# Kernel optimization log

Measured on AMD Instinct MI355X. Metric: run time of the kernel, lower is better.

The kernel has to match this reference:

```python
import jax, jax.numpy as jnp
import numpy as np

N = 20000      # nodes
E = 320000     # edges (avg degree 16)
NODE_DIM = 64
EDGE_DIM = 32
HID = 128
HEADS = 4
NEG_SLOPE = 0.2


def _gatv2(x, src, dst, edge_attr, Wl, bl, Wr, br, We, att, bias, heads, out_ch):
    """PyG GATv2Conv (concat=True). x:[N,F], src/dst:[E], edge_attr:[E,edge_dim]."""
    n = x.shape[0]
    xl = (x @ Wl + bl).reshape(n, heads, out_ch)          # source transform
    xr = (x @ Wr + br).reshape(n, heads, out_ch)          # target transform
    ee = (edge_attr @ We).reshape(-1, heads, out_ch)      # edge embedding (no bias in PyG)
    m = jax.nn.leaky_relu(xl[src] + xr[dst] + ee, NEG_SLOPE)  # [E,H,C]
    logits = jnp.einsum('ehc,hc->eh', m, att)             # [E,H]
    # segment softmax over incoming edges of each destination node
    lmax = jax.ops.segment_max(logits, dst, num_segments=n)
    ex = jnp.exp(logits - lmax[dst])
    denom = jax.ops.segment_sum(ex, dst, num_segments=n)
    alpha = ex / denom[dst]                               # [E,H]
    out = jax.ops.segment_sum(alpha[..., None] * xl[src], dst, num_segments=n)
    return out.reshape(n, heads * out_ch) + bias


def setup_inputs() -> dict:
    key = jax.random.key(0)
    ks = jax.random.split(key, 24)
    d = {}
    d['x'] = jax.random.normal(ks[0], (N, NODE_DIM), jnp.float32)
    d['edge_index'] = jax.random.randint(ks[1], (2, E), 0, N, jnp.int64)
    d['edge_attr'] = jax.random.normal(ks[2], (E, EDGE_DIM), jnp.float32)
    HC1 = HEADS * HID
    def lin(k, fi, fo):
        return jax.random.normal(k, (fi, fo), jnp.float32) / np.sqrt(fi).astype(np.float32)
    # conv1: node_dim -> hid, heads=4
    d['Wl1'] = lin(ks[3], NODE_DIM, HC1); d['bl1'] = jnp.zeros((HC1,), jnp.float32)
    d['Wr1'] = lin(ks[4], NODE_DIM, HC1); d['br1'] = jnp.zeros((HC1,), jnp.float32)
    d['We1'] = lin(ks[5], EDGE_DIM, HC1)
    d['att1'] = jax.random.normal(ks[6], (HEADS, HID), jnp.float32) / np.sqrt(HID).astype(np.float32)
    d['bias1'] = jnp.zeros((HC1,), jnp.float32)
    # conv2: hid*heads -> hid, heads=1
    d['Wl2'] = lin(ks[7], HC1, HID); d['bl2'] = jnp.zeros((HID,), jnp.float32)
    d['Wr2'] = lin(ks[8], HC1, HID); d['br2'] = jnp.zeros((HID,), jnp.float32)
    d['We2'] = lin(ks[9], EDGE_DIM, HID)
    d['att2'] = jax.random.normal(ks[10], (1, HID), jnp.float32) / np.sqrt(HID).astype(np.float32)
    d['bias2'] = jnp.zeros((HID,), jnp.float32)
    # stereo head
    d['Wh1'] = lin(ks[11], HID, 64); d['bh1'] = jnp.zeros((64,), jnp.float32)
    d['Wh2'] = lin(ks[12], 64, 2);   d['bh2'] = jnp.zeros((2,), jnp.float32)
    return d


def reference(x, edge_index, edge_attr, Wl1, bl1, Wr1, br1, We1, att1, bias1,
              Wl2, bl2, Wr2, br2, We2, att2, bias2, Wh1, bh1, Wh2, bh2):
    src, dst = edge_index[0], edge_index[1]
    h = _gatv2(x, src, dst, edge_attr, Wl1, bl1, Wr1, br1, We1, att1, bias1, HEADS, HID)
    h = jax.nn.relu(h)
    h = _gatv2(h, src, dst, edge_attr, Wl2, bl2, Wr2, br2, We2, att2, bias2, 1, HID)
    h = jax.nn.relu(h @ Wh1 + bh1)
    return h @ Wh2 + bh2  # [N, 2]
```

## Files before the change

kernel.cpp:

```cpp
#include <hip/hip_runtime.h>
#include <hip/hip_bf16.h>
#include <math.h>

#define N_NODES 20000
#define N_EDGES 320000
#define NODE_DIM 64
#define EDGE_DIM 32
#define HID 128
#define HEADS 4
#define HC1 512
#define NEG_SLOPE 0.2f

typedef __attribute__((ext_vector_type(8))) short bf16x8;
typedef __attribute__((ext_vector_type(4))) float f32x4;

__device__ __forceinline__ unsigned short f2b(float f) {
  __hip_bfloat16 h = __float2bfloat16(f);
  unsigned short s;
  __builtin_memcpy(&s, &h, 2);
  return s;
}
__device__ __forceinline__ float b2f(unsigned short b) {
  return __uint_as_float(((unsigned)b) << 16);
}

__global__ void deg_count_kernel(const int* __restrict__ dsts, int* __restrict__ deg) {
  int e = blockIdx.x * blockDim.x + threadIdx.x;
  if (e < N_EDGES) atomicAdd(&deg[dsts[e]], 1);
}

__global__ __launch_bounds__(1024) void scan_kernel(
    const int* __restrict__ deg, int* __restrict__ offs, int* __restrict__ cursor)
{
  __shared__ int part[1024];
  int t = threadIdx.x;
  const int C = 20;
  int base = t * C;
  int loc[C]; int s = 0;
  #pragma unroll
  for (int i = 0; i < C; i++) { loc[i] = s; int idx = base + i; s += (idx < N_NODES) ? deg[idx] : 0; }
  part[t] = s;
  __syncthreads();
  for (int off = 1; off < 1024; off <<= 1) {
    int v = (t >= off) ? part[t - off] : 0;
    __syncthreads();
    part[t] += v;
    __syncthreads();
  }
  int pbase = (t > 0) ? part[t - 1] : 0;
  #pragma unroll
  for (int i = 0; i < C; i++) {
    int idx = base + i;
    if (idx < N_NODES) { int o = pbase + loc[i]; offs[idx] = o; cursor[idx] = o; }
  }
  if (t == 1023) offs[N_NODES] = part[1023];
}

__global__ void scatter_kernel(const int* __restrict__ dsts, int* __restrict__ cursor,
                               int* __restrict__ csr) {
  int e = blockIdx.x * blockDim.x + threadIdx.x;
  if (e >= N_EDGES) return;
  int pos = atomicAdd(&cursor[dsts[e]], 1);
  csr[pos] = e;
}

__global__ void wconv_kernel(const float* __restrict__ Wl1, const float* __restrict__ Wr1,
                             const float* __restrict__ Wl2, const float* __restrict__ Wr2,
                             unsigned short* __restrict__ WT1, unsigned short* __restrict__ WT2)
{
  int i = blockIdx.x * blockDim.x + threadIdx.x;
  if (i < 1024 * 64) {
    int col = i >> 6, k = i & 63;
    float v = (col < 512) ? Wl1[(size_t)k * HC1 + col] : Wr1[(size_t)k * HC1 + col - 512];
    WT1[i] = f2b(v);
  }
  if (i < 256 * 512) {
    int col = i >> 9, k = i & 511;
    float v = (col < 128) ? Wl2[(size_t)k * HID + col] : Wr2[(size_t)k * HID + col - 128];
    WT2[i] = f2b(v);
  }
}

__global__ __launch_bounds__(256, 4) void linear1_kernel(
    const float* __restrict__ x, const unsigned short* __restrict__ WT1,
    const float* __restrict__ bl, const float* __restrict__ br,
    float* __restrict__ xl, float* __restrict__ xr)
{
  __shared__ short xs[16 * 72];
  int t = threadIdx.x;
  int n0 = blockIdx.x * 16;
  {
    int i = t * 4;
    int node = i >> 6, k = i & 63;
    float4 v = *(const float4*)&x[(size_t)(n0 + node) * NODE_DIM + k];
    short* d = &xs[node * 72 + k];
    d[0] = (short)f2b(v.x); d[1] = (short)f2b(v.y);
    d[2] = (short)f2b(v.z); d[3] = (short)f2b(v.w);
  }
  __syncthreads();
  int wave = t >> 6, lane = t & 63;
  int l15 = lane & 15, l16 = lane >> 4;
  bf16x8 a0 = *(bf16x8*)&xs[l15 * 72 + 0  + l16 * 8];
  bf16x8 a1 = *(bf16x8*)&xs[l15 * 72 + 32 + l16 * 8];
  #pragma unroll 4
  for (int tt = 0; tt < 16; tt++) {
    int col = wave * 256 + tt * 16 + l15;
    const unsigned short* wp = &WT1[(size_t)col * 64 + l16 * 8];
    bf16x8 b0 = *(bf16x8*)&wp[0];
    bf16x8 b1 = *(bf16x8*)&wp[32];
    f32x4 acc = {0.f, 0.f, 0.f, 0.f};
    acc = __builtin_amdgcn_mfma_f32_16x16x32_bf16(a0, b0, acc, 0, 0, 0);
    acc = __builtin_amdgcn_mfma_f32_16x16x32_bf16(a1, b1, acc, 0, 0, 0);
    float bv = (col < 512) ? bl[col] : br[col - 512];
    float* outp = (col < 512) ? xl : xr;
    int cc = (col < 512) ? col : col - 512;
    #pragma unroll
    for (int r = 0; r < 4; r++)
      outp[(size_t)(n0 + l16 * 4 + r) * HC1 + cc] = acc[r] + bv;
  }
}

__global__ __launch_bounds__(1024, 2) void fused1_kernel(
    const float* __restrict__ ea, const int* __restrict__ srcs,
    const float* __restrict__ We, const float* __restrict__ att,
    const float* __restrict__ xl, const float* __restrict__ xr,
    const float* __restrict__ bias, const int* __restrict__ offs,
    const int* __restrict__ csr, unsigned short* __restrict__ h1b)
{
  __shared__ short WtT[256 * 40];
  __shared__ short easb[16][16 * 40];
  __shared__ short ee_b[16][8][136];
  int t = threadIdx.x;
  int half = blockIdx.x & 1;
  for (int i = t; i < EDGE_DIM * 256; i += 1024) {
    int k = i >> 8, c = i & 255;
    WtT[c * 40 + k] = (short)f2b(We[(size_t)k * HC1 + half * 256 + c]);
  }
  __syncthreads();
  int wave = t >> 6, lane = t & 63;
  int l15 = lane & 15, l16 = lane >> 4;
  int n = (blockIdx.x >> 1) * 16 + wave;
  int Cl = lane * 4;
  int C = half * 256 + Cl;
  bool phA = (Cl < 128);
  int Cm = Cl & 127;
  float at4[4], xr4[4];
  *(float4*)at4 = *(const float4*)&att[C];
  *(float4*)xr4 = *(const float4*)&xr[(size_t)n * HC1 + C];
  float o4[4] = {0.f,0.f,0.f,0.f};
  float mx = 8.0f, dn = 0.f;
  int beg = offs[n], end = offs[n + 1];
  int ev = 0, sv = 0;
  if (lane < 8 && beg + lane < end) { ev = csr[beg + lane]; sv = srcs[ev]; }
  for (int i0 = beg; i0 < end; i0 += 8) {
    int nv = end - i0; if (nv > 8) nv = 8;
    int sarr[8];
    #pragma unroll
    for (int j = 0; j < 8; j++) sarr[j] = __shfl(sv, j);
    float xv[8][4];
    #pragma unroll
    for (int j = 0; j < 8; j++) {
      if (j < nv) *(float4*)&xv[j][0] = *(const float4*)&xl[(size_t)sarr[j] * HC1 + C];
      else { xv[j][0] = 0.f; xv[j][1] = 0.f; xv[j][2] = 0.f; xv[j][3] = 0.f; }
    }
    {
      int me = __shfl(ev, lane >> 2);
      if (lane < 32) {
        int q = lane & 3;
        float4 u0 = *(const float4*)&ea[(size_t)me * EDGE_DIM + q * 8];
        float4 u1 = *(const float4*)&ea[(size_t)me * EDGE_DIM + q * 8 + 4];
        short* dst = &easb[wave][(lane >> 2) * 40 + q * 8];
        dst[0] = (short)f2b(u0.x); dst[1] = (short)f2b(u0.y);
        dst[2] = (short)f2b(u0.z); dst[3] = (short)f2b(u0.w);
        dst[4] = (short)f2b(u1.x); dst[5] = (short)f2b(u1.y);
        dst[6] = (short)f2b(u1.z); dst[7] = (short)f2b(u1.w);
      }
    }
    if (lane < 8 && i0 + 8 + lane < end) { ev = csr[i0 + 8 + lane]; sv = srcs[ev]; }
    bf16x8 bfrag = *(bf16x8*)&easb[wave][l15 * 40 + l16 * 8];
    float pl[8];
    #pragma unroll 4
    for (int tt = 0; tt < 8; tt++) {
      bf16x8 afrag = *(bf16x8*)&WtT[(tt * 16 + l15) * 40 + l16 * 8];
      f32x4 cz = {0.f, 0.f, 0.f, 0.f};
      f32x4 cv = __builtin_amdgcn_mfma_f32_16x16x32_bf16(afrag, bfrag, cz, 0, 0, 0);
      if (l15 < 8) {
        ushort4 u;
        u.x = f2b(cv[0]); u.y = f2b(cv[1]); u.z = f2b(cv[2]); u.w = f2b(cv[3]);
        *(ushort4*)&ee_b[wave][l15][tt * 16 + l16 * 4] = u;
      }
    }
    #pragma unroll
    for (int j = 0; j < 8; j++) {
      float s = 0.f;
      if (phA) {
        ushort4 ub = *(const ushort4*)&ee_b[wave][j][Cm];
        float z0 = b2f(ub.x) + xv[j][0] + xr4[0];
        float z1 = b2f(ub.y) + xv[j][1] + xr4[1];
        float z2 = b2f(ub.z) + xv[j][2] + xr4[2];
        float z3 = b2f(ub.w) + xv[j][3] + xr4[3];
        z0 = z0 > 0.f ? z0 : NEG_SLOPE * z0;
        z1 = z1 > 0.f ? z1 : NEG_SLOPE * z1;
        z2 = z2 > 0.f ? z2 : NEG_SLOPE * z2;
        z3 = z3 > 0.f ? z3 : NEG_SLOPE * z3;
        s = ((z0 * at4[0] + z1 * at4[1]) + (z2 * at4[2] + z3 * at4[3]));
      }
      pl[j] = s;
    }
    #pragma unroll 4
    for (int tt = 8; tt < 16; tt++) {
      bf16x8 afrag = *(bf16x8*)&WtT[(tt * 16 + l15) * 40 + l16 * 8];
      f32x4 cz = {0.f, 0.f, 0.f, 0.f};
      f32x4 cv = __builtin_amdgcn_mfma_f32_16x16x32_bf16(afrag, bfrag, cz, 0, 0, 0);
      if (l15 < 8) {
        ushort4 u;
        u.x = f2b(cv[0]); u.y = f2b(cv[1]); u.z = f2b(cv[2]); u.w = f2b(cv[3]);
        *(ushort4*)&ee_b[wave][l15][(tt - 8) * 16 + l16 * 4] = u;
      }
    }
    #pragma unroll
    for (int j = 0; j < 8; j++) {
      if (!phA) {
        ushort4 ub = *(const ushort4*)&ee_b[wave][j][Cm];
        float z0 = b2f(ub.x) + xv[j][0] + xr4[0];
        float z1 = b2f(ub.y) + xv[j][1] + xr4[1];
        float z2 = b2f(ub.z) + xv[j][2] + xr4[2];
        float z3 = b2f(ub.w) + xv[j][3] + xr4[3];
        z0 = z0 > 0.f ? z0 : NEG_SLOPE * z0;
        z1 = z1 > 0.f ? z1 : NEG_SLOPE * z1;
        z2 = z2 > 0.f ? z2 : NEG_SLOPE * z2;
        z3 = z3 > 0.f ? z3 : NEG_SLOPE * z3;
        pl[j] = ((z0 * at4[0] + z1 * at4[1]) + (z2 * at4[2] + z3 * at4[3]));
      }
    }
    #pragma unroll
    for (int j = 0; j < 8; j++) {
      float s = pl[j];
      #pragma unroll
      for (int o = 1; o <= 16; o <<= 1) s += __shfl_xor(s, o);
      pl[j] = (j < nv) ? s : -3.0e38f;
    }
    float cm = fmaxf(fmaxf(fmaxf(pl[0], pl[1]), fmaxf(pl[2], pl[3])),
                     fmaxf(fmaxf(pl[4], pl[5]), fmaxf(pl[6], pl[7])));
    float mn = fmaxf(mx, cm);
    if (__any(mn > mx + 8.f)) {
      float fs = __expf(mx - mn);
      dn *= fs;
      #pragma unroll
      for (int c = 0; c < 4; c++) o4[c] *= fs;
      mx = mn;
    }
    float p[8];
    #pragma unroll
    for (int j = 0; j < 8; j++) p[j] = __expf(pl[j] - mx);
    dn += ((p[0] + p[1]) + (p[2] + p[3])) + ((p[4] + p[5]) + (p[6] + p[7]));
    #pragma unroll
    for (int c = 0; c < 4; c++) {
      float acc = 0.f;
      #pragma unroll
      for (int j = 0; j < 8; j++) acc = fmaf(p[j], xv[j][c], acc);
      o4[c] += acc;
    }
  }
  float iv = dn > 0.f ? 1.f / dn : 0.f;
  ushort4 u;
  float v0 = o4[0] * iv + bias[C + 0]; v0 = v0 > 0.f ? v0 : 0.f;
  float v1 = o4[1] * iv + bias[C + 1]; v1 = v1 > 0.f ? v1 : 0.f;
  float v2 = o4[2] * iv + bias[C + 2]; v2 = v2 > 0.f ? v2 : 0.f;
  float v3 = o4[3] * iv + bias[C + 3]; v3 = v3 > 0.f ? v3 : 0.f;
  u.x = f2b(v0); u.y = f2b(v1); u.z = f2b(v2); u.w = f2b(v3);
  *(ushort4*)&h1b[(size_t)n * HC1 + C] = u;
}

__global__ __launch_bounds__(256, 4) void linear2_kernel(
    const unsigned short* __restrict__ hin, const unsigned short* __restrict__ WT2,
    const float* __restrict__ bl, const float* __restrict__ br,
    float* __restrict__ xl2, float* __restrict__ xr2)
{
  __shared__ short hs[16 * 520];
  int t = threadIdx.x;
  int n0 = blockIdx.x * 16;
  for (int rr = 0; rr < 8; rr++) {
    int i = (t + rr * 256) * 4;
    int node = i >> 9, k = i & 511;
    short* d = &hs[node * 520 + k];
    ushort4 u = *(const ushort4*)&hin[(size_t)(n0 + node) * HC1 + k];
    d[0] = (short)u.x; d[1] = (short)u.y; d[2] = (short)u.z; d[3] = (short)u.w;
  }
  __syncthreads();
  int wave = t >> 6, lane = t & 63;
  int l15 = lane & 15, l16 = lane >> 4;
  f32x4 acc0 = {0.f,0.f,0.f,0.f}, acc1 = {0.f,0.f,0.f,0.f};
  f32x4 acc2 = {0.f,0.f,0.f,0.f}, acc3 = {0.f,0.f,0.f,0.f};
  int colb = wave * 64 + l15;
  #pragma unroll 2
  for (int ks = 0; ks < 16; ks++) {
    bf16x8 a = *(bf16x8*)&hs[l15 * 520 + ks * 32 + l16 * 8];
    bf16x8 b0 = *(bf16x8*)&WT2[(size_t)(colb +  0) * 512 + ks * 32 + l16 * 8];
    bf16x8 b1 = *(bf16x8*)&WT2[(size_t)(colb + 16) * 512 + ks * 32 + l16 * 8];
    bf16x8 b2 = *(bf16x8*)&WT2[(size_t)(colb + 32) * 512 + ks * 32 + l16 * 8];
    bf16x8 b3 = *(bf16x8*)&WT2[(size_t)(colb + 48) * 512 + ks * 32 + l16 * 8];
    acc0 = __builtin_amdgcn_mfma_f32_16x16x32_bf16(a, b0, acc0, 0, 0, 0);
    acc1 = __builtin_amdgcn_mfma_f32_16x16x32_bf16(a, b1, acc1, 0, 0, 0);
    acc2 = __builtin_amdgcn_mfma_f32_16x16x32_bf16(a, b2, acc2, 0, 0, 0);
    acc3 = __builtin_amdgcn_mfma_f32_16x16x32_bf16(a, b3, acc3, 0, 0, 0);
  }
  #pragma unroll
  for (int tt = 0; tt < 4; tt++) {
    const f32x4* ap = (tt == 0) ? &acc0 : (tt == 1) ? &acc1 : (tt == 2) ? &acc2 : &acc3;
    int col = wave * 64 + tt * 16 + l15;
    float bv = (col < 128) ? bl[col] : br[col - 128];
    float* outp = (col < 128) ? xl2 : xr2;
    int cc = (col < 128) ? col : col - 128;
    #pragma unroll
    for (int r = 0; r < 4; r++)
      outp[(size_t)(n0 + l16 * 4 + r) * HID + cc] = (*ap)[r] + bv;
  }
}

__global__ __launch_bounds__(512, 2) void fused2_kernel(
    const float* __restrict__ ea, const int* __restrict__ srcs,
    const float* __restrict__ We, const float* __restrict__ att,
    const float* __restrict__ xl, const float* __restrict__ xr,
    const float* __restrict__ bias, const int* __restrict__ offs,
    const int* __restrict__ csr, float* __restrict__ h2out)
{
  __shared__ short W2tT[HID * 40];
  __shared__ short easb2[8][16 * 40];
  __shared__ short ee2b[8][16][136];
  int t = threadIdx.x;
  for (int i = t; i < EDGE_DIM * HID; i += 512) {
    int k = i >> 7, c = i & 127;
    W2tT[c * 40 + k] = (short)f2b(We[(size_t)k * HID + c]);
  }
  __syncthreads();
  int wave = t >> 6, lane = t & 63;
  int l15 = lane & 15, l16 = lane >> 4;
  int n = blockIdx.x * 8 + wave;
  int c = lane * 2;
  float2 atv = *(const float2*)&att[c];
  float2 xrv = *(const float2*)&xr[(size_t)n * HID + c];
  float oa = 0.f, ob = 0.f;
  float m = 8.0f, d = 0.f;
  int beg = offs[n], end = offs[n + 1];
  int ev = 0, sv = 0;
  if (lane < 16 && beg + lane < end) { ev = csr[beg + lane]; sv = srcs[ev]; }
  for (int i0 = beg; i0 < end; i0 += 16) {
    int nv = end - i0; if (nv > 16) nv = 16;
    int sarr[16];
    #pragma unroll
    for (int j = 0; j < 16; j++) sarr[j] = __shfl(sv, j);
    float2 xv[16];
    #pragma unroll
    for (int j = 0; j < 16; j++) {
      if (j < nv) xv[j] = *(const float2*)&xl[(size_t)sarr[j] * HID + c];
      else { xv[j].x = 0.f; xv[j].y = 0.f; }
    }
    {
      int me = __shfl(ev, lane >> 2);
      int q = lane & 3;
      float4 u0 = *(const float4*)&ea[(size_t)me * EDGE_DIM + q * 8];
      float4 u1 = *(const float4*)&ea[(size_t)me * EDGE_DIM + q * 8 + 4];
      short* dst = &easb2[wave][(lane >> 2) * 40 + q * 8];
      dst[0] = (short)f2b(u0.x); dst[1] = (short)f2b(u0.y);
      dst[2] = (short)f2b(u0.z); dst[3] = (short)f2b(u0.w);
      dst[4] = (short)f2b(u1.x); dst[5] = (short)f2b(u1.y);
      dst[6] = (short)f2b(u1.z); dst[7] = (short)f2b(u1.w);
    }
    if (lane < 16 && i0 + 16 + lane < end) { ev = csr[i0 + 16 + lane]; sv = srcs[ev]; }
    bf16x8 bfrag = *(bf16x8*)&easb2[wave][l15 * 40 + l16 * 8];
    #pragma unroll 4
    for (int tt = 0; tt < 8; tt++) {
      bf16x8 afrag = *(bf16x8*)&W2tT[(tt * 16 + l15) * 40 + l16 * 8];
      f32x4 cz = {0.f, 0.f, 0.f, 0.f};
      f32x4 cv = __builtin_amdgcn_mfma_f32_16x16x32_bf16(afrag, bfrag, cz, 0, 0, 0);
      ushort4 u;
      u.x = f2b(cv[0]); u.y = f2b(cv[1]); u.z = f2b(cv[2]); u.w = f2b(cv[3]);
      *(ushort4*)&ee2b[wave][l15][tt * 16 + l16 * 4] = u;
    }
    float pl[16];
    #pragma unroll
    for (int j = 0; j < 16; j++) {
      ushort2 uv = *(const ushort2*)&ee2b[wave][j][c];
      float za = b2f(uv.x) + xv[j].x + xrv.x;
      float zb = b2f(uv.y) + xv[j].y + xrv.y;
      za = za > 0.f ? za : NEG_SLOPE * za;
      zb = zb > 0.f ? zb : NEG_SLOPE * zb;
      float s = za * atv.x + zb * atv.y;
      #pragma unroll
      for (int o = 1; o < 64; o <<= 1) s += __shfl_xor(s, o);
      pl[j] = (j < nv) ? s : -3.0e38f;
    }
    float cm = pl[0];
    #pragma unroll
    for (int j = 1; j < 16; j++) cm = fmaxf(cm, pl[j]);
    float mn = fmaxf(m, cm);
    if (__any(mn > m + 8.f)) {
      float fs = __expf(m - mn);
      d *= fs; oa *= fs; ob *= fs;
      m = mn;
    }
    #pragma unroll
    for (int j = 0; j < 16; j++) {
      float p = __expf(pl[j] - m);
      d += p;
      oa = fmaf(p, xv[j].x, oa);
      ob = fmaf(p, xv[j].y, ob);
    }
  }
  float invd = d > 0.f ? 1.f / d : 0.f;
  float2 o2 = make_float2(oa * invd + bias[c], ob * invd + bias[c + 1]);
  *(float2*)&h2out[(size_t)n * HID + c] = o2;
}

__global__ __launch_bounds__(256) void head_kernel(
    const float* __restrict__ h2, const float* __restrict__ Wh1,
    const float* __restrict__ bh1, const float* __restrict__ Wh2,
    const float* __restrict__ bh2, float* __restrict__ out)
{
  __shared__ float hs[16][HID];
  __shared__ float ts[16][64];
  int n0 = blockIdx.x * 16;
  int t = threadIdx.x;
  for (int r = 0; r < 2; r++) {
    int flat = (t + r * 256) * 4;
    int i = flat >> 7, k = flat & 127;
    *(float4*)&hs[i][k] = *(const float4*)&h2[(size_t)(n0 + i) * HID + k];
  }
  __syncthreads();
  int j = t & 63, g = t >> 6;
  float acc[4];
  #pragma unroll
  for (int q = 0; q < 4; q++) acc[q] = 0.f;
  for (int k = 0; k < HID; k++) {
    float w = Wh1[k * 64 + j];
    #pragma unroll
    for (int q = 0; q < 4; q++) acc[q] = fmaf(hs[g + 4 * q][k], w, acc[q]);
  }
  float bj = bh1[j];
  #pragma unroll
  for (int q = 0; q < 4; q++) {
    float v = acc[q] + bj;
    ts[g + 4 * q][j] = v > 0.f ? v : 0.f;
  }
  __syncthreads();
  if (t < 32) {
    int nl = t >> 1, k = t & 1;
    float acc2 = bh2[k];
    for (int jj = 0; jj < 64; jj++) acc2 = fmaf(ts[nl][jj], Wh2[jj * 2 + k], acc2);
    out[(size_t)(n0 + nl) * 2 + k] = acc2;
  }
}

extern "C" void kernel_launch(void* const* d_in, const int* in_sizes, int n_in,
                              void* d_out, int out_size, void* d_ws, size_t ws_size,
                              hipStream_t stream)
{
  (void)in_sizes; (void)n_in; (void)out_size; (void)ws_size;
  const float* x    = (const float*)d_in[0];
  const int* eidx   = (const int*)d_in[1];
  const float* ea   = (const float*)d_in[2];
  const float* Wl1  = (const float*)d_in[3];
  const float* bl1  = (const float*)d_in[4];
  const float* Wr1  = (const float*)d_in[5];
  const float* br1  = (const float*)d_in[6];
  const float* We1  = (const float*)d_in[7];
  const float* att1 = (const float*)d_in[8];
  const float* bias1= (const float*)d_in[9];
  const float* Wl2  = (const float*)d_in[10];
  const float* bl2  = (const float*)d_in[11];
  const float* Wr2  = (const float*)d_in[12];
  const float* br2  = (const float*)d_in[13];
  const float* We2  = (const float*)d_in[14];
  const float* att2 = (const float*)d_in[15];
  const float* bias2= (const float*)d_in[16];
  const float* Wh1  = (const float*)d_in[17];
  const float* bh1  = (const float*)d_in[18];
  const float* Wh2  = (const float*)d_in[19];
  const float* bh2  = (const float*)d_in[20];
  const int* srcs = eidx;
  const int* dsts = eidx + N_EDGES;
  float* out = (float*)d_out;

  char* p = (char*)d_ws;
  auto alloc = [&](size_t bytes) { char* q = p; p += (bytes + 511) & ~(size_t)511; return q; };
  float*          xl1  = (float*)alloc((size_t)N_NODES * HC1 * 4);
  float*          xr1  = (float*)alloc((size_t)N_NODES * HC1 * 4);
  unsigned short* h1b  = (unsigned short*)alloc((size_t)N_NODES * HC1 * 2);
  int* deg    = (int*)alloc((size_t)N_NODES * 4);
  int* offs   = (int*)alloc((size_t)(N_NODES + 1) * 4);
  int* cursor = (int*)alloc((size_t)N_NODES * 4);
  int* csr    = (int*)alloc((size_t)N_EDGES * 4);
  unsigned short* WT1 = (unsigned short*)alloc(1024 * 64 * 2);
  unsigned short* WT2 = (unsigned short*)alloc(256 * 512 * 2);
  float* xl2 = xl1;
  float* xr2 = xl1 + (size_t)N_NODES * HID;
  float* h2  = xl1 + (size_t)2 * N_NODES * HID;

  hipMemsetAsync(deg, 0, (size_t)N_NODES * 4, stream);
  hipLaunchKernelGGL(deg_count_kernel, dim3((N_EDGES + 255) / 256), dim3(256), 0, stream, dsts, deg);
  hipLaunchKernelGGL(wconv_kernel, dim3(512), dim3(256), 0, stream, Wl1, Wr1, Wl2, Wr2, WT1, WT2);
  hipLaunchKernelGGL(scan_kernel, dim3(1), dim3(1024), 0, stream, deg, offs, cursor);
  hipLaunchKernelGGL(scatter_kernel, dim3((N_EDGES + 255) / 256), dim3(256), 0, stream, dsts, cursor, csr);
  hipLaunchKernelGGL(linear1_kernel, dim3(N_NODES / 16), dim3(256), 0, stream,
                     x, WT1, bl1, br1, xl1, xr1);
  hipLaunchKernelGGL(fused1_kernel, dim3((N_NODES / 16) * 2), dim3(1024), 0, stream,
                     ea, srcs, We1, att1, xl1, xr1, bias1, offs, csr, h1b);
  hipLaunchKernelGGL(linear2_kernel, dim3(N_NODES / 16), dim3(256), 0, stream,
                     h1b, WT2, bl2, br2, xl2, xr2);
  hipLaunchKernelGGL(fused2_kernel, dim3(N_NODES / 8), dim3(512), 0, stream,
                     ea, srcs, We2, att2, xl2, xr2, bias2, offs, csr, h2);
  hipLaunchKernelGGL(head_kernel, dim3(N_NODES / 16), dim3(256), 0, stream,
                     h2, Wh1, bh1, Wh2, bh2, out);
}
```

Baseline: 411.1 us.

## Process four destination nodes per wave to amortize shared weight staging

Both fused attention kernels now loop over four destination nodes per wave instead of one, so the block-level conversion of the edge weight matrix into shared memory is amortized over more nodes and fewer blocks are launched. fused1 also shrinks to 512 threads and widens its edge-embedding scratch buffer so all 16 MFMA tiles are computed in one pass, removing the split two-phase schedule. The trade-off is fewer blocks, less parallelism, and serialized per-node work within each wave, which may expose more gather latency and load imbalance.

```diff
diff --git a/kernel.cpp b/kernel.cpp
--- a/kernel.cpp
+++ b/kernel.cpp
@@ -120,7 +120,7 @@
   }
 }
 
-__global__ __launch_bounds__(1024, 2) void fused1_kernel(
+__global__ __launch_bounds__(512, 2) void fused1_kernel(
     const float* __restrict__ ea, const int* __restrict__ srcs,
     const float* __restrict__ We, const float* __restrict__ att,
     const float* __restrict__ xl, const float* __restrict__ xr,
@@ -128,73 +128,72 @@
     const int* __restrict__ csr, unsigned short* __restrict__ h1b)
 {
   __shared__ short WtT[256 * 40];
-  __shared__ short easb[16][16 * 40];
-  __shared__ short ee_b[16][8][136];
+  __shared__ short easb[8][16 * 40];
+  __shared__ short ee_b[8][8][264];
   int t = threadIdx.x;
   int half = blockIdx.x & 1;
-  for (int i = t; i < EDGE_DIM * 256; i += 1024) {
+  for (int i = t; i < EDGE_DIM * 256; i += 512) {
     int k = i >> 8, c = i & 255;
     WtT[c * 40 + k] = (short)f2b(We[(size_t)k * HC1 + half * 256 + c]);
   }
   __syncthreads();
   int wave = t >> 6, lane = t & 63;
   int l15 = lane & 15, l16 = lane >> 4;
-  int n = (blockIdx.x >> 1) * 16 + wave;
+  int nbase = (blockIdx.x >> 1) * 32 + wave * 4;
   int Cl = lane * 4;
   int C = half * 256 + Cl;
-  bool phA = (Cl < 128);
-  int Cm = Cl & 127;
-  float at4[4], xr4[4];
+  float at4[4];
   *(float4*)at4 = *(const float4*)&att[C];
-  *(float4*)xr4 = *(const float4*)&xr[(size_t)n * HC1 + C];
-  float o4[4] = {0.f,0.f,0.f,0.f};
-  float mx = 8.0f, dn = 0.f;
-  int beg = offs[n], end = offs[n + 1];
-  int ev = 0, sv = 0;
-  if (lane < 8 && beg + lane < end) { ev = csr[beg + lane]; sv = srcs[ev]; }
-  for (int i0 = beg; i0 < end; i0 += 8) {
-    int nv = end - i0; if (nv > 8) nv = 8;
-    int sarr[8];
-    #pragma unroll
-    for (int j = 0; j < 8; j++) sarr[j] = __shfl(sv, j);
-    float xv[8][4];
-    #pragma unroll
-    for (int j = 0; j < 8; j++) {
-      if (j < nv) *(float4*)&xv[j][0] = *(const float4*)&xl[(size_t)sarr[j] * HC1 + C];
-      else { xv[j][0] = 0.f; xv[j][1] = 0.f; xv[j][2] = 0.f; xv[j][3] = 0.f; }
-    }
-    {
-      int me = __shfl(ev, lane >> 2);
-      if (lane < 32) {
-        int q = lane & 3;
-        float4 u0 = *(const float4*)&ea[(size_t)me * EDGE_DIM + q * 8];
-        float4 u1 = *(const float4*)&ea[(size_t)me * EDGE_DIM + q * 8 + 4];
-        short* dst = &easb[wave][(lane >> 2) * 40 + q * 8];
-        dst[0] = (short)f2b(u0.x); dst[1] = (short)f2b(u0.y);
-        dst[2] = (short)f2b(u0.z); dst[3] = (short)f2b(u0.w);
-        dst[4] = (short)f2b(u1.x); dst[5] = (short)f2b(u1.y);
-        dst[6] = (short)f2b(u1.z); dst[7] = (short)f2b(u1.w);
-      }
-    }
-    if (lane < 8 && i0 + 8 + lane < end) { ev = csr[i0 + 8 + lane]; sv = srcs[ev]; }
-    bf16x8 bfrag = *(bf16x8*)&easb[wave][l15 * 40 + l16 * 8];
-    float pl[8];
-    #pragma unroll 4
-    for (int tt = 0; tt < 8; tt++) {
-      bf16x8 afrag = *(bf16x8*)&WtT[(tt * 16 + l15) * 40 + l16 * 8];
-      f32x4 cz = {0.f, 0.f, 0.f, 0.f};
-      f32x4 cv = __builtin_amdgcn_mfma_f32_16x16x32_bf16(afrag, bfrag, cz, 0, 0, 0);
-      if (l15 < 8) {
-        ushort4 u;
-        u.x = f2b(cv[0]); u.y = f2b(cv[1]); u.z = f2b(cv[2]); u.w = f2b(cv[3]);
-        *(ushort4*)&ee_b[wave][l15][tt * 16 + l16 * 4] = u;
-      }
-    }
-    #pragma unroll
-    for (int j = 0; j < 8; j++) {
-      float s = 0.f;
-      if (phA) {
-        ushort4 ub = *(const ushort4*)&ee_b[wave][j][Cm];
+  for (int nn = 0; nn < 4; nn++) {
+    int n = nbase + nn;
+    float xr4[4];
+    *(float4*)xr4 = *(const float4*)&xr[(size_t)n * HC1 + C];
+    float o4[4] = {0.f,0.f,0.f,0.f};
+    float mx = 8.0f, dn = 0.f;
+    int beg = offs[n], end = offs[n + 1];
+    int ev = 0, sv = 0;
+    if (lane < 8 && beg + lane < end) { ev = csr[beg + lane]; sv = srcs[ev]; }
+    for (int i0 = beg; i0 < end; i0 += 8) {
+      int nv = end - i0; if (nv > 8) nv = 8;
+      int sarr[8];
+      #pragma unroll
+      for (int j = 0; j < 8; j++) sarr[j] = __shfl(sv, j);
+      float xv[8][4];
+      #pragma unroll
+      for (int j = 0; j < 8; j++) {
+        if (j < nv) *(float4*)&xv[j][0] = *(const float4*)&xl[(size_t)sarr[j] * HC1 + C];
+        else { xv[j][0] = 0.f; xv[j][1] = 0.f; xv[j][2] = 0.f; xv[j][3] = 0.f; }
+      }
+      {
+        int me = __shfl(ev, lane >> 2);
+        if (lane < 32) {
+          int q = lane & 3;
+          float4 u0 = *(const float4*)&ea[(size_t)me * EDGE_DIM + q * 8];
+          float4 u1 = *(const float4*)&ea[(size_t)me * EDGE_DIM + q * 8 + 4];
+          short* dst = &easb[wave][(lane >> 2) * 40 + q * 8];
+          dst[0] = (short)f2b(u0.x); dst[1] = (short)f2b(u0.y);
+          dst[2] = (short)f2b(u0.z); dst[3] = (short)f2b(u0.w);
+          dst[4] = (short)f2b(u1.x); dst[5] = (short)f2b(u1.y);
+          dst[6] = (short)f2b(u1.z); dst[7] = (short)f2b(u1.w);
+        }
+      }
+      if (lane < 8 && i0 + 8 + lane < end) { ev = csr[i0 + 8 + lane]; sv = srcs[ev]; }
+      bf16x8 bfrag = *(bf16x8*)&easb[wave][l15 * 40 + l16 * 8];
+      #pragma unroll 4
+      for (int tt = 0; tt < 16; tt++) {
+        bf16x8 afrag = *(bf16x8*)&WtT[(tt * 16 + l15) * 40 + l16 * 8];
+        f32x4 cz = {0.f, 0.f, 0.f, 0.f};
+        f32x4 cv = __builtin_amdgcn_mfma_f32_16x16x32_bf16(afrag, bfrag, cz, 0, 0, 0);
+        if (l15 < 8) {
+          ushort4 u;
+          u.x = f2b(cv[0]); u.y = f2b(cv[1]); u.z = f2b(cv[2]); u.w = f2b(cv[3]);
+          *(ushort4*)&ee_b[wave][l15][tt * 16 + l16 * 4] = u;
+        }
+      }
+      float pl[8];
+      #pragma unroll
+      for (int j = 0; j < 8; j++) {
+        ushort4 ub = *(const ushort4*)&ee_b[wave][j][Cl];
         float z0 = b2f(ub.x) + xv[j][0] + xr4[0];
         float z1 = b2f(ub.y) + xv[j][1] + xr4[1];
         float z2 = b2f(ub.z) + xv[j][2] + xr4[2];
@@ -203,73 +202,42 @@
         z1 = z1 > 0.f ? z1 : NEG_SLOPE * z1;
         z2 = z2 > 0.f ? z2 : NEG_SLOPE * z2;
         z3 = z3 > 0.f ? z3 : NEG_SLOPE * z3;
-        s = ((z0 * at4[0] + z1 * at4[1]) + (z2 * at4[2] + z3 * at4[3]));
-      }
-      pl[j] = s;
+        float s = ((z0 * at4[0] + z1 * at4[1]) + (z2 * at4[2] + z3 * at4[3]));
+        #pragma unroll
+        for (int o = 1; o <= 16; o <<= 1) s += __shfl_xor(s, o);
+        pl[j] = (j < nv) ? s : -3.0e38f;
+      }
+      float cm = fmaxf(fmaxf(fmaxf(pl[0], pl[1]), fmaxf(pl[2], pl[3])),
+                       fmaxf(fmaxf(pl[4], pl[5]), fmaxf(pl[6], pl[7])));
+      float mn = fmaxf(mx, cm);
+      if (__any(mn > mx + 8.f)) {
+        float fs = __expf(mx - mn);
+        dn *= fs;
+        #pragma unroll
+        for (int c = 0; c < 4; c++) o4[c] *= fs;
+        mx = mn;
+      }
+      float p[8];
+      #pragma unroll
+      for (int j = 0; j < 8; j++) p[j] = __expf(pl[j] - mx);
+      dn += ((p[0] + p[1]) + (p[2] + p[3])) + ((p[4] + p[5]) + (p[6] + p[7]));
+      #pragma unroll
+      for (int c = 0; c < 4; c++) {
+        float acc = 0.f;
+        #pragma unroll
+        for (int j = 0; j < 8; j++) acc = fmaf(p[j], xv[j][c], acc);
+        o4[c] += acc;
+      }
     }
-    #pragma unroll 4
-    for (int tt = 8; tt < 16; tt++) {
-      bf16x8 afrag = *(bf16x8*)&WtT[(tt * 16 + l15) * 40 + l16 * 8];
-      f32x4 cz = {0.f, 0.f, 0.f, 0.f};
-      f32x4 cv = __builtin_amdgcn_mfma_f32_16x16x32_bf16(afrag, bfrag, cz, 0, 0, 0);
-      if (l15 < 8) {
-        ushort4 u;
-        u.x = f2b(cv[0]); u.y = f2b(cv[1]); u.z = f2b(cv[2]); u.w = f2b(cv[3]);
-        *(ushort4*)&ee_b[wave][l15][(tt - 8) * 16 + l16 * 4] = u;
-      }
-    }
-    #pragma unroll
-    for (int j = 0; j < 8; j++) {
-      if (!phA) {
-        ushort4 ub = *(const ushort4*)&ee_b[wave][j][Cm];
-        float z0 = b2f(ub.x) + xv[j][0] + xr4[0];
-        float z1 = b2f(ub.y) + xv[j][1] + xr4[1];
-        float z2 = b2f(ub.z) + xv[j][2] + xr4[2];
-        float z3 = b2f(ub.w) + xv[j][3] + xr4[3];
-        z0 = z0 > 0.f ? z0 : NEG_SLOPE * z0;
-        z1 = z1 > 0.f ? z1 : NEG_SLOPE * z1;
-        z2 = z2 > 0.f ? z2 : NEG_SLOPE * z2;
-        z3 = z3 > 0.f ? z3 : NEG_SLOPE * z3;
-        pl[j] = ((z0 * at4[0] + z1 * at4[1]) + (z2 * at4[2] + z3 * at4[3]));
-      }
-    }
-    #pragma unroll
-    for (int j = 0; j < 8; j++) {
-      float s = pl[j];
-      #pragma unroll
-      for (int o = 1; o <= 16; o <<= 1) s += __shfl_xor(s, o);
-      pl[j] = (j < nv) ? s : -3.0e38f;
-    }
-    float cm = fmaxf(fmaxf(fmaxf(pl[0], pl[1]), fmaxf(pl[2], pl[3])),
-                     fmaxf(fmaxf(pl[4], pl[5]), fmaxf(pl[6], pl[7])));
-    float mn = fmaxf(mx, cm);
-    if (__any(mn > mx + 8.f)) {
-      float fs = __expf(mx - mn);
-      dn *= fs;
-      #pragma unroll
-      for (int c = 0; c < 4; c++) o4[c] *= fs;
-      mx = mn;
-    }
-    float p[8];
-    #pragma unroll
-    for (int j = 0; j < 8; j++) p[j] = __expf(pl[j] - mx);
-    dn += ((p[0] + p[1]) + (p[2] + p[3])) + ((p[4] + p[5]) + (p[6] + p[7]));
-    #pragma unroll
-    for (int c = 0; c < 4; c++) {
-      float acc = 0.f;
-      #pragma unroll
-      for (int j = 0; j < 8; j++) acc = fmaf(p[j], xv[j][c], acc);
-      o4[c] += acc;
-    }
-  }
-  float iv = dn > 0.f ? 1.f / dn : 0.f;
-  ushort4 u;
-  float v0 = o4[0] * iv + bias[C + 0]; v0 = v0 > 0.f ? v0 : 0.f;
-  float v1 = o4[1] * iv + bias[C + 1]; v1 = v1 > 0.f ? v1 : 0.f;
-  float v2 = o4[2] * iv + bias[C + 2]; v2 = v2 > 0.f ? v2 : 0.f;
-  float v3 = o4[3] * iv + bias[C + 3]; v3 = v3 > 0.f ? v3 : 0.f;
-  u.x = f2b(v0); u.y = f2b(v1); u.z = f2b(v2); u.w = f2b(v3);
-  *(ushort4*)&h1b[(size_t)n * HC1 + C] = u;
+    float iv = dn > 0.f ? 1.f / dn : 0.f;
+    ushort4 u;
+    float v0 = o4[0] * iv + bias[C + 0]; v0 = v0 > 0.f ? v0 : 0.f;
+    float v1 = o4[1] * iv + bias[C + 1]; v1 = v1 > 0.f ? v1 : 0.f;
+    float v2 = o4[2] * iv + bias[C + 2]; v2 = v2 > 0.f ? v2 : 0.f;
+    float v3 = o4[3] * iv + bias[C + 3]; v3 = v3 > 0.f ? v3 : 0.f;
+    u.x = f2b(v0); u.y = f2b(v1); u.z = f2b(v2); u.w = f2b(v3);
+    *(ushort4*)&h1b[(size_t)n * HC1 + C] = u;
+  }
 }
 
 __global__ __launch_bounds__(256, 4) void linear2_kernel(
@@ -336,81 +304,84 @@
   __syncthreads();
   int wave = t >> 6, lane = t & 63;
   int l15 = lane & 15, l16 = lane >> 4;
-  int n = blockIdx.x * 8 + wave;
+  int nbase = blockIdx.x * 32 + wave * 4;
   int c = lane * 2;
   float2 atv = *(const float2*)&att[c];
-  float2 xrv = *(const float2*)&xr[(size_t)n * HID + c];
-  float oa = 0.f, ob = 0.f;
-  float m = 8.0f, d = 0.f;
-  int beg = offs[n], end = offs[n + 1];
-  int ev = 0, sv = 0;
-  if (lane < 16 && beg + lane < end) { ev = csr[beg + lane]; sv = srcs[ev]; }
-  for (int i0 = beg; i0 < end; i0 += 16) {
-    int nv = end - i0; if (nv > 16) nv = 16;
-    int sarr[16];
-    #pragma unroll
-    for (int j = 0; j < 16; j++) sarr[j] = __shfl(sv, j);
-    float2 xv[16];
-    #pragma unroll
-    for (int j = 0; j < 16; j++) {
-      if (j < nv) xv[j] = *(const float2*)&xl[(size_t)sarr[j] * HID + c];
-      else { xv[j].x = 0.f; xv[j].y = 0.f; }
+  for (int nn = 0; nn < 4; nn++) {
+    int n = nbase + nn;
+    float2 xrv = *(const float2*)&xr[(size_t)n * HID + c];
+    float oa = 0.f, ob = 0.f;
+    float m = 8.0f, d = 0.f;
+    int beg = offs[n], end = offs[n + 1];
+    int ev = 0, sv = 0;
+    if (lane < 16 && beg + lane < end) { ev = csr[beg + lane]; sv = srcs[ev]; }
+    for (int i0 = beg; i0 < end; i0 += 16) {
+      int nv = end - i0; if (nv > 16) nv = 16;
+      int sarr[16];
+      #pragma unroll
+      for (int j = 0; j < 16; j++) sarr[j] = __shfl(sv, j);
+      float2 xv[16];
+      #pragma unroll
+      for (int j = 0; j < 16; j++) {
+        if (j < nv) xv[j] = *(const float2*)&xl[(size_t)sarr[j] * HID + c];
+        else { xv[j].x = 0.f; xv[j].y = 0.f; }
+      }
+      {
+        int me = __shfl(ev, lane >> 2);
+        int q = lane & 3;
+        float4 u0 = *(const float4*)&ea[(size_t)me * EDGE_DIM + q * 8];
+        float4 u1 = *(const float4*)&ea[(size_t)me * EDGE_DIM + q * 8 + 4];
+        short* dst = &easb2[wave][(lane >> 2) * 40 + q * 8];
+        dst[0] = (short)f2b(u0.x); dst[1] = (short)f2b(u0.y);
+        dst[2] = (short)f2b(u0.z); dst[3] = (short)f2b(u0.w);
+        dst[4] = (short)f2b(u1.x); dst[5] = (short)f2b(u1.y);
+        dst[6] = (short)f2b(u1.z); dst[7] = (short)f2b(u1.w);
+      }
+      if (lane < 16 && i0 + 16 + lane < end) { ev = csr[i0 + 16 + lane]; sv = srcs[ev]; }
+      bf16x8 bfrag = *(bf16x8*)&easb2[wave][l15 * 40 + l16 * 8];
+      #pragma unroll 4
+      for (int tt = 0; tt < 8; tt++) {
+        bf16x8 afrag = *(bf16x8*)&W2tT[(tt * 16 + l15) * 40 + l16 * 8];
+        f32x4 cz = {0.f, 0.f, 0.f, 0.f};
+        f32x4 cv = __builtin_amdgcn_mfma_f32_16x16x32_bf16(afrag, bfrag, cz, 0, 0, 0);
+        ushort4 u;
+        u.x = f2b(cv[0]); u.y = f2b(cv[1]); u.z = f2b(cv[2]); u.w = f2b(cv[3]);
+        *(ushort4*)&ee2b[wave][l15][tt * 16 + l16 * 4] = u;
+      }
+      float pl[16];
+      #pragma unroll
+      for (int j = 0; j < 16; j++) {
+        ushort2 uv = *(const ushort2*)&ee2b[wave][j][c];
+        float za = b2f(uv.x) + xv[j].x + xrv.x;
+        float zb = b2f(uv.y) + xv[j].y + xrv.y;
+        za = za > 0.f ? za : NEG_SLOPE * za;
+        zb = zb > 0.f ? zb : NEG_SLOPE * zb;
+        float s = za * atv.x + zb * atv.y;
+        #pragma unroll
+        for (int o = 1; o < 64; o <<= 1) s += __shfl_xor(s, o);
+        pl[j] = (j < nv) ? s : -3.0e38f;
+      }
+      float cm = pl[0];
+      #pragma unroll
+      for (int j = 1; j < 16; j++) cm = fmaxf(cm, pl[j]);
+      float mn = fmaxf(m, cm);
+      if (__any(mn > m + 8.f)) {
+        float fs = __expf(m - mn);
+        d *= fs; oa *= fs; ob *= fs;
+        m = mn;
+      }
+      #pragma unroll
+      for (int j = 0; j < 16; j++) {
+        float p = __expf(pl[j] - m);
+        d += p;
+        oa = fmaf(p, xv[j].x, oa);
+        ob = fmaf(p, xv[j].y, ob);
+      }
     }
-    {
-      int me = __shfl(ev, lane >> 2);
-      int q = lane & 3;
-      float4 u0 = *(const float4*)&ea[(size_t)me * EDGE_DIM + q * 8];
-      float4 u1 = *(const float4*)&ea[(size_t)me * EDGE_DIM + q * 8 + 4];
-      short* dst = &easb2[wave][(lane >> 2) * 40 + q * 8];
-      dst[0] = (short)f2b(u0.x); dst[1] = (short)f2b(u0.y);
-      dst[2] = (short)f2b(u0.z); dst[3] = (short)f2b(u0.w);
-      dst[4] = (short)f2b(u1.x); dst[5] = (short)f2b(u1.y);
-      dst[6] = (short)f2b(u1.z); dst[7] = (short)f2b(u1.w);
-    }
-    if (lane < 16 && i0 + 16 + lane < end) { ev = csr[i0 + 16 + lane]; sv = srcs[ev]; }
-    bf16x8 bfrag = *(bf16x8*)&easb2[wave][l15 * 40 + l16 * 8];
-    #pragma unroll 4
-    for (int tt = 0; tt < 8; tt++) {
-      bf16x8 afrag = *(bf16x8*)&W2tT[(tt * 16 + l15) * 40 + l16 * 8];
-      f32x4 cz = {0.f, 0.f, 0.f, 0.f};
-      f32x4 cv = __builtin_amdgcn_mfma_f32_16x16x32_bf16(afrag, bfrag, cz, 0, 0, 0);
-      ushort4 u;
-      u.x = f2b(cv[0]); u.y = f2b(cv[1]); u.z = f2b(cv[2]); u.w = f2b(cv[3]);
-      *(ushort4*)&ee2b[wave][l15][tt * 16 + l16 * 4] = u;
-    }
-    float pl[16];
-    #pragma unroll
-    for (int j = 0; j < 16; j++) {
-      ushort2 uv = *(const ushort2*)&ee2b[wave][j][c];
-      float za = b2f(uv.x) + xv[j].x + xrv.x;
-      float zb = b2f(uv.y) + xv[j].y + xrv.y;
-      za = za > 0.f ? za : NEG_SLOPE * za;
-      zb = zb > 0.f ? zb : NEG_SLOPE * zb;
-      float s = za * atv.x + zb * atv.y;
-      #pragma unroll
-      for (int o = 1; o < 64; o <<= 1) s += __shfl_xor(s, o);
-      pl[j] = (j < nv) ? s : -3.0e38f;
-    }
-    float cm = pl[0];
-    #pragma unroll
-    for (int j = 1; j < 16; j++) cm = fmaxf(cm, pl[j]);
-    float mn = fmaxf(m, cm);
-    if (__any(mn > m + 8.f)) {
-      float fs = __expf(m - mn);
-      d *= fs; oa *= fs; ob *= fs;
-      m = mn;
-    }
-    #pragma unroll
-    for (int j = 0; j < 16; j++) {
-      float p = __expf(pl[j] - m);
-      d += p;
-      oa = fmaf(p, xv[j].x, oa);
-      ob = fmaf(p, xv[j].y, ob);
-    }
-  }
-  float invd = d > 0.f ? 1.f / d : 0.f;
-  float2 o2 = make_float2(oa * invd + bias[c], ob * invd + bias[c + 1]);
-  *(float2*)&h2out[(size_t)n * HID + c] = o2;
+    float invd = d > 0.f ? 1.f / d : 0.f;
+    float2 o2 = make_float2(oa * invd + bias[c], ob * invd + bias[c + 1]);
+    *(float2*)&h2out[(size_t)n * HID + c] = o2;
+  }
 }
 
 __global__ __launch_bounds__(256) void head_kernel(
@@ -504,11 +475,11 @@
   hipLaunchKernelGGL(scatter_kernel, dim3((N_EDGES + 255) / 256), dim3(256), 0, stream, dsts, cursor, csr);
   hipLaunchKernelGGL(linear1_kernel, dim3(N_NODES / 16), dim3(256), 0, stream,
                      x, WT1, bl1, br1, xl1, xr1);
-  hipLaunchKernelGGL(fused1_kernel, dim3((N_NODES / 16) * 2), dim3(1024), 0, stream,
+  hipLaunchKernelGGL(fused1_kernel, dim3((N_NODES / 32) * 2), dim3(512), 0, stream,
                      ea, srcs, We1, att1, xl1, xr1, bias1, offs, csr, h1b);
   hipLaunchKernelGGL(linear2_kernel, dim3(N_NODES / 16), dim3(256), 0, stream,
                      h1b, WT2, bl2, br2, xl2, xr2);
-  hipLaunchKernelGGL(fused2_kernel, dim3(N_NODES / 8), dim3(512), 0, stream,
+  hipLaunchKernelGGL(fused2_kernel, dim3(N_NODES / 32), dim3(512), 0, stream,
                      ea, srcs, We2, att2, xl2, xr2, bias2, offs, csr, h2);
   hipLaunchKernelGGL(head_kernel, dim3(N_NODES / 16), dim3(256), 0, stream,
                      h2, Wh1, bh1, Wh2, bh2, out);
```

New measurement: 381.2 us. 1.08x faster.
